# Kernel tuning notes

Hardware: AMD Instinct MI355X
Metric: run time of the kernel (lower is better)

## Reference

```python
import jax, jax.numpy as jnp
import numpy as np

NUM_EMBEDDINGS = 1024
EMBEDDING_DIM = 64
COMMITMENT_COST = 0.25


def setup_inputs() -> dict:
    key = jax.random.key(0)
    k1, k2 = jax.random.split(key)
    inputs = jax.random.normal(k1, (64, 32, 32, EMBEDDING_DIM), dtype=jnp.float32)
    embeddings = jax.random.normal(k2, (NUM_EMBEDDINGS, EMBEDDING_DIM), dtype=jnp.float32)
    return {"inputs": inputs, "embeddings": embeddings}


def reference(inputs, embeddings):
    # flatten spatial dims: [B, HW, D]
    flat = jnp.reshape(inputs, (inputs.shape[0], -1, EMBEDDING_DIM))
    distances = (
        jnp.sum(flat ** 2, axis=2, keepdims=True)
        - 2.0 * jnp.einsum("btd,kd->btk", flat, embeddings)
        + jnp.sum(embeddings ** 2, axis=1)
    )
    encoding_indices = jnp.argmin(distances, axis=2)  # [B, HW]
    # direct gather == one-hot @ embeddings, same math, no [B,HW,K] one-hot
    quantized = jnp.take(embeddings, encoding_indices, axis=0)  # [B, HW, D]
    quantized = jnp.reshape(quantized, inputs.shape)
    e_latent_loss = jnp.mean((jax.lax.stop_gradient(quantized) - inputs) ** 2)
    loss = COMMITMENT_COST * e_latent_loss
    quantized = inputs + jax.lax.stop_gradient(quantized - inputs)
    return quantized, loss, encoding_indices
```

## Files before the change

### kernel.cpp

```cpp
#include <hip/hip_runtime.h>

#define D 64
#define NK 1024
#define QTOTAL 65536
#define NELEM (QTOTAL * D)
#define LOSS_OFF 4194304
#define IDX_OUT_OFF 4194305
#define CAPQ 16384
#define MARGIN 2.0e-3f

typedef float f32x16 __attribute__((ext_vector_type(16)));
typedef short bf16x8 __attribute__((ext_vector_type(8)));
typedef float f32x4 __attribute__((ext_vector_type(4)));
typedef unsigned int u32;
typedef unsigned short ushort_t;

#define WS_E2   0
#define WS_B    4096
#define WS_CNT  266240
#define WS_LIST 266496
#define WS_NEED 332032

__device__ __forceinline__ ushort_t f2bf(float f) {
    u32 u = __float_as_uint(f);
    return (ushort_t)((u + 0x7FFFu + ((u >> 16) & 1u)) >> 16);
}
__device__ __forceinline__ float bf2f(ushort_t h) {
    return __uint_as_float(((u32)h) << 16);
}

__global__ __launch_bounds__(256) void vqk0(const float* __restrict__ emb,
                                            u32* __restrict__ b32,
                                            float* __restrict__ e2, u32* __restrict__ cnt,
                                            float* __restrict__ out) {
    int gid = blockIdx.x * 256 + threadIdx.x;
    int c = gid >> 5;
    int d = (gid & 31) * 2;
    float2 v = ((const float2*)emb)[gid];
    ushort_t h0 = f2bf(v.x), h1 = f2bf(v.y);
    ushort_t m0 = f2bf(v.x - bf2f(h0)), m1 = f2bf(v.y - bf2f(h1));
    int t = c >> 4, row = c & 15;
    int g = (d & 31) >> 3;
    int bh = (d < 32) ? 0 : 1;
    int lane = g * 16 + row;
    int u = t * 1024 + lane * 4 + ((d & 7) >> 1);
    b32[u + bh * 256]       = (u32)h0 | ((u32)h1 << 16);
    b32[u + (bh + 2) * 256] = (u32)m0 | ((u32)m1 << 16);
    if (gid < NK) {
        const float4* e4 = (const float4*)(emb + (long)gid * D);
        float s = 0.f;
#pragma unroll
        for (int i = 0; i < D / 4; ++i) {
            float4 w = e4[i];
            s += w.x * w.x + w.y * w.y + w.z * w.z + w.w * w.w;
        }
        e2[gid] = s;
    }
    if (gid == 0) { out[LOSS_OFF] = 0.0f; *cnt = 0; }
}

#define LDB(P) (*(const bf16x8*)(P))

#define COMPUTE_TILE(T, BH0, BH1, BM0, BM1) do {                               \
    const int c_ = (T) * 16 + row;                                             \
    const float h_ = 0.5f * e2l[c_];                                           \
    _Pragma("unroll")                                                          \
    for (int s_ = 0; s_ < 2; ++s_) {                                           \
        f32x4 acc = {0.f, 0.f, 0.f, 0.f};                                      \
        acc = __builtin_amdgcn_mfma_f32_16x16x32_bf16(ah[s_][0], BM0, acc, 0, 0, 0); \
        acc = __builtin_amdgcn_mfma_f32_16x16x32_bf16(am[s_][0], BH0, acc, 0, 0, 0); \
        acc = __builtin_amdgcn_mfma_f32_16x16x32_bf16(ah[s_][0], BH0, acc, 0, 0, 0); \
        acc = __builtin_amdgcn_mfma_f32_16x16x32_bf16(ah[s_][1], BM1, acc, 0, 0, 0); \
        acc = __builtin_amdgcn_mfma_f32_16x16x32_bf16(am[s_][1], BH1, acc, 0, 0, 0); \
        acc = __builtin_amdgcn_mfma_f32_16x16x32_bf16(ah[s_][1], BH1, acc, 0, 0, 0); \
        _Pragma("unroll")                                                      \
        for (int r_ = 0; r_ < 4; ++r_) {                                       \
            int sl_ = s_ * 4 + r_;                                             \
            float sd_ = h_ - acc[r_];                                          \
            float ns2_ = fminf(fmaxf(sd_, s1v[sl_]), s2v[sl_]);      \
            bool lt_ = sd_ < s1v[sl_];                                         \
            i1v[sl_] = lt_ ? c_ : i1v[sl_];                                    \
            s1v[sl_] = fminf(sd_, s1v[sl_]);                                   \
            s2v[sl_] = ns2_;                                                   \
        }                                                                      \
    }                                                                          \
} while (0)

__global__ __launch_bounds__(256, 2) void vqk1(const float* __restrict__ x,
                                               const ushort_t* __restrict__ B,
                                               const float* __restrict__ e2g,
                                               const float* __restrict__ emb,
                                               u32* __restrict__ cnt,
                                               int* __restrict__ list,
                                               float* __restrict__ out) {
    __shared__ float e2l[NK];
    __shared__ int   idx_l[128];
    __shared__ float lred[4];

    const int tid = threadIdx.x;
    const int l = tid & 63;
    const int w = tid >> 6;
    const int qbase = blockIdx.x * 128;
    const int wb = qbase + w * 32;
    const int row = l & 15;
    const int g = l >> 4;
    const int koff = g * 8;

    ((f32x4*)e2l)[tid] = ((const f32x4*)e2g)[tid];

    bf16x8 ah[2][2], am[2][2];
#pragma unroll
    for (int s = 0; s < 2; ++s) {
        const float* xr = x + (long)(wb + s * 16 + row) * D + koff;
#pragma unroll
        for (int half = 0; half < 2; ++half) {
            float4 p0 = ((const float4*)(xr + half * 32))[0];
            float4 p1 = ((const float4*)(xr + half * 32))[1];
            float v[8] = {p0.x, p0.y, p0.z, p0.w, p1.x, p1.y, p1.z, p1.w};
#pragma unroll
            for (int i = 0; i < 8; ++i) {
                ushort_t hs = f2bf(v[i]);
                ushort_t ms = f2bf(v[i] - bf2f(hs));
                ah[s][half][i] = (short)hs;
                am[s][half][i] = (short)ms;
            }
        }
    }
    __syncthreads();

    float s1v[8], s2v[8];
    int i1v[8];
#pragma unroll
    for (int i = 0; i < 8; ++i) { s1v[i] = 3.4e38f; s2v[i] = 3.4e38f; i1v[i] = 0; }

    int off = l * 8;
    bf16x8 bh0 = LDB(B + off),        bh1 = LDB(B + off + 512);
    bf16x8 bm0 = LDB(B + off + 1024), bm1 = LDB(B + off + 1536);
#pragma unroll 1
    for (int t = 0; t < 64; t += 2) {
        int o1 = off + 2048;
        bf16x8 ch0 = LDB(B + o1),        ch1 = LDB(B + o1 + 512);
        bf16x8 cm0 = LDB(B + o1 + 1024), cm1 = LDB(B + o1 + 1536);
        COMPUTE_TILE(t, bh0, bh1, bm0, bm1);
        int o2 = (t == 62) ? (l * 8) : (off + 4096);
        bh0 = LDB(B + o2);        bh1 = LDB(B + o2 + 512);
        bm0 = LDB(B + o2 + 1024); bm1 = LDB(B + o2 + 1536);
        COMPUTE_TILE(t + 1, ch0, ch1, cm0, cm1);
        off = o2;
    }

#pragma unroll
    for (int d = 1; d < 16; d <<= 1) {
#pragma unroll
        for (int sl = 0; sl < 8; ++sl) {
            float os1 = __shfl_xor(s1v[sl], d, 64);
            float os2 = __shfl_xor(s2v[sl], d, 64);
            int   oi1 = __shfl_xor(i1v[sl], d, 64);
            float hi = s1v[sl] > os1 ? s1v[sl] : os1;
            float lo2 = s2v[sl] < os2 ? s2v[sl] : os2;
            int ni = (os1 < s1v[sl]) ? oi1
                   : ((os1 == s1v[sl] && oi1 < i1v[sl]) ? oi1 : i1v[sl]);
            s1v[sl] = s1v[sl] < os1 ? s1v[sl] : os1;
            s2v[sl] = hi < lo2 ? hi : lo2;
            i1v[sl] = ni;
        }
    }

    if (row == 0) {
#pragma unroll
        for (int sl = 0; sl < 8; ++sl) {
            int s = sl >> 2, r = sl & 3;
            int ql = w * 32 + s * 16 + g * 4 + r;
            idx_l[ql] = i1v[sl];
            if (s2v[sl] - s1v[sl] <= MARGIN) {
                u32 p = atomicAdd(cnt, 1u);
                if (p < CAPQ) list[p] = qbase + ql;
            }
        }
    }
    __syncthreads();

    if (l < 32) out[IDX_OUT_OFF + wb + l] = (float)idx_l[w * 32 + l];

    const f32x4* x4 = (const f32x4*)(x + (long)wb * D);
    const f32x4* e4 = (const f32x4*)emb;
    f32x4* o4 = (f32x4*)(out + (long)wb * D);
    float ls = 0.f;
#pragma unroll 1
    for (int k = 0; k < 8; ++k) {
        int j = l + 64 * k;
        int ql = j >> 4;
        int col = j & 15;
        int idx = idx_l[w * 32 + ql];
        f32x4 xv = x4[j];
        f32x4 ev = e4[idx * 16 + col];
        o4[j] = ev;
        f32x4 dd = ev - xv;
        ls += dd[0] * dd[0] + dd[1] * dd[1] + dd[2] * dd[2] + dd[3] * dd[3];
    }
#pragma unroll
    for (int offr = 32; offr > 0; offr >>= 1) ls += __shfl_down(ls, offr, 64);
    if (l == 0) lred[w] = ls;
    __syncthreads();
    if (tid == 0)
        atomicAdd(&out[LOSS_OFF],
                  (lred[0] + lred[1] + lred[2] + lred[3]) * (0.25f / (float)NELEM));
}

__global__ __launch_bounds__(64) void vqk2(const float* __restrict__ x,
                                           const float* __restrict__ emb,
                                           const float* __restrict__ e2,
                                           const int* __restrict__ list,
                                           const u32* __restrict__ cnt,
                                           float* __restrict__ out) {
    u32 n = *cnt; if (n > CAPQ) n = CAPQ;
    const int l = threadIdx.x;
    for (u32 f = blockIdx.x; f < n; f += gridDim.x) {
        int q = list[f];
        float4 xv[16];
        const float4* xp = (const float4*)(x + (long)q * D);
#pragma unroll
        for (int i = 0; i < 16; ++i) xv[i] = xp[i];
        float best = 3.4e38f; int bi = 0;
#pragma unroll 1
        for (int i = 0; i < 16; ++i) {
            int c = l * 16 + i;
            const float4* ep = (const float4*)(emb + (long)c * D);
            float a0 = 0.f, a1 = 0.f, a2 = 0.f, a3 = 0.f;
#pragma unroll
            for (int k = 0; k < 16; ++k) {
                float4 e = ep[k];
                a0 = fmaf(e.x, xv[k].x, a0); a1 = fmaf(e.y, xv[k].y, a1);
                a2 = fmaf(e.z, xv[k].z, a2); a3 = fmaf(e.w, xv[k].w, a3);
            }
            float s = 0.5f * e2[c] - ((a0 + a1) + (a2 + a3));
            if (s < best) { best = s; bi = c; }
        }
#pragma unroll
        for (int off = 32; off > 0; off >>= 1) {
            float ob = __shfl_down(best, off, 64);
            int   oi = __shfl_down(bi, off, 64);
            if (ob < best || (ob == best && oi < bi)) { best = ob; bi = oi; }
        }
        bi = __shfl(bi, 0, 64);
        int ci = (int)out[IDX_OUT_OFF + q];
        if (bi != ci) {
            float xl = x[(long)q * D + l];
            float en = emb[(long)bi * D + l];
            float eo = emb[(long)ci * D + l];
            out[(long)q * D + l] = en;
            float dn = (en - xl) * (en - xl);
            float dol = (eo - xl) * (eo - xl);
            float dd = dn - dol;
#pragma unroll
            for (int off = 32; off > 0; off >>= 1) dd += __shfl_down(dd, off, 64);
            if (l == 0) {
                out[IDX_OUT_OFF + q] = (float)bi;
                atomicAdd(&out[LOSS_OFF], dd * (0.25f / (float)NELEM));
            }
        }
    }
}

#define FDO_CHUNK(B, K) \
    aA0 = fmaf(B[0],  xA[4*K+0].x, aA0); aA1 = fmaf(B[1],  xA[4*K+0].y, aA1); \
    aA2 = fmaf(B[2],  xA[4*K+0].z, aA2); aA3 = fmaf(B[3],  xA[4*K+0].w, aA3); \
    aA0 = fmaf(B[4],  xA[4*K+1].x, aA0); aA1 = fmaf(B[5],  xA[4*K+1].y, aA1); \
    aA2 = fmaf(B[6],  xA[4*K+1].z, aA2); aA3 = fmaf(B[7],  xA[4*K+1].w, aA3); \
    aA0 = fmaf(B[8],  xA[4*K+2].x, aA0); aA1 = fmaf(B[9],  xA[4*K+2].y, aA1); \
    aA2 = fmaf(B[10], xA[4*K+2].z, aA2); aA3 = fmaf(B[11], xA[4*K+2].w, aA3); \
    aA0 = fmaf(B[12], xA[4*K+3].x, aA0); aA1 = fmaf(B[13], xA[4*K+3].y, aA1); \
    aA2 = fmaf(B[14], xA[4*K+3].z, aA2); aA3 = fmaf(B[15], xA[4*K+3].w, aA3); \
    aB0 = fmaf(B[0],  xB[4*K+0].x, aB0); aB1 = fmaf(B[1],  xB[4*K+0].y, aB1); \
    aB2 = fmaf(B[2],  xB[4*K+0].z, aB2); aB3 = fmaf(B[3],  xB[4*K+0].w, aB3); \
    aB0 = fmaf(B[4],  xB[4*K+1].x, aB0); aB1 = fmaf(B[5],  xB[4*K+1].y, aB1); \
    aB2 = fmaf(B[6],  xB[4*K+1].z, aB2); aB3 = fmaf(B[7],  xB[4*K+1].w, aB3); \
    aB0 = fmaf(B[8],  xB[4*K+2].x, aB0); aB1 = fmaf(B[9],  xB[4*K+2].y, aB1); \
    aB2 = fmaf(B[10], xB[4*K+2].z, aB2); aB3 = fmaf(B[11], xB[4*K+2].w, aB3); \
    aB0 = fmaf(B[12], xB[4*K+3].x, aB0); aB1 = fmaf(B[13], xB[4*K+3].y, aB1); \
    aB2 = fmaf(B[14], xB[4*K+3].z, aB2); aB3 = fmaf(B[15], xB[4*K+3].w, aB3);

__global__ __launch_bounds__(256) void vq_e2f(const float* __restrict__ emb,
                                              float* __restrict__ e2,
                                              float* __restrict__ out) {
    int k = blockIdx.x * blockDim.x + threadIdx.x;
    if (k == 0) out[LOSS_OFF] = 0.0f;
    if (k < NK) {
        const float4* e4 = (const float4*)(emb + k * D);
        float s = 0.f;
#pragma unroll
        for (int i = 0; i < D / 4; ++i) {
            float4 v = e4[i];
            s += v.x * v.x + v.y * v.y + v.z * v.z + v.w * v.w;
        }
        e2[k] = s;
    }
}

__global__ __launch_bounds__(256, 2) void vq_mainf(const float* __restrict__ x,
                                                   const float* __restrict__ emb,
                                                   const float* __restrict__ e2g,
                                                   float* __restrict__ out) {
    __shared__ float e2l[NK];
    __shared__ float sm_s[512];
    __shared__ int   sm_c[512];
    const int tid = threadIdx.x;
    const int l = tid & 63;
    const int w = tid >> 6;
    const int qbase = blockIdx.x * 128;
    ((float4*)e2l)[tid] = ((const float4*)e2g)[tid];
    float4 xA[16], xB[16];
    const float4* xpA = (const float4*)(x + (long)(qbase + l) * D);
    const float4* xpB = (const float4*)(x + (long)(qbase + 64 + l) * D);
#pragma unroll
    for (int i = 0; i < 16; ++i) { xA[i] = xpA[i]; xB[i] = xpB[i]; }
    __syncthreads();
    const int code0 = __builtin_amdgcn_readfirstlane(w << 8);
    const float* ep0 = emb + (long)code0 * D;
    float bestA = 3.4e38f, bestB = 3.4e38f;
    int idxA = 0, idxB = 0;
#pragma unroll 1
    for (int g = 0; g < 256; ++g) {
        const float* ep = ep0 + g * D;
        f32x16 b0, b1, b2, b3;
        asm volatile(
            "s_load_dwordx16 %0, %4, 0x0\n\t"
            "s_load_dwordx16 %1, %4, 0x40\n\t"
            "s_load_dwordx16 %2, %4, 0x80\n\t"
            "s_load_dwordx16 %3, %4, 0xC0\n\t"
            "s_waitcnt lgkmcnt(0)"
            : "=s"(b0), "=s"(b1), "=s"(b2), "=s"(b3) : "s"(ep));
        float aA0 = 0.f, aA1 = 0.f, aA2 = 0.f, aA3 = 0.f;
        float aB0 = 0.f, aB1 = 0.f, aB2 = 0.f, aB3 = 0.f;
        FDO_CHUNK(b0, 0) FDO_CHUNK(b1, 1) FDO_CHUNK(b2, 2) FDO_CHUNK(b3, 3)
        float dotA = (aA0 + aA1) + (aA2 + aA3);
        float dotB = (aB0 + aB1) + (aB2 + aB3);
        float e2c = e2l[code0 + g];
        float sA = 0.5f * e2c - dotA;
        float sB = 0.5f * e2c - dotB;
        int code = code0 + g;
        bool lt;
        lt = sA < bestA; bestA = lt ? sA : bestA; idxA = lt ? code : idxA;
        lt = sB < bestB; bestB = lt ? sB : bestB; idxB = lt ? code : idxB;
    }
    sm_s[w * 128 + l] = bestA;      sm_c[w * 128 + l] = idxA;
    sm_s[w * 128 + 64 + l] = bestB; sm_c[w * 128 + 64 + l] = idxB;
    __syncthreads();
    if (tid < 128) {
        float bs = sm_s[tid]; int bc = sm_c[tid];
#pragma unroll
        for (int wv = 1; wv < 4; ++wv) {
            float s = sm_s[wv * 128 + tid]; int c = sm_c[wv * 128 + tid];
            if (s < bs) { bs = s; bc = c; }
        }
        const int q = qbase + tid;
        out[IDX_OUT_OFF + q] = (float)bc;
        const float4* eb = (const float4*)(emb + (long)bc * D);
        const float4* xq = (const float4*)(x + (long)q * D);
        float4* oq = (float4*)(out + (long)q * D);
        float lsum = 0.f;
#pragma unroll
        for (int i = 0; i < 16; ++i) {
            float4 e = eb[i]; float4 xx = xq[i];
            oq[i] = e;
            float dx = e.x - xx.x, dy = e.y - xx.y, dz = e.z - xx.z, dw = e.w - xx.w;
            lsum += dx * dx + dy * dy + dz * dz + dw * dw;
        }
#pragma unroll
        for (int o = 32; o > 0; o >>= 1) lsum += __shfl_down(lsum, o, 64);
        if ((tid & 63) == 0) atomicAdd(&out[LOSS_OFF], lsum * (0.25f / (float)NELEM));
    }
}

extern "C" void kernel_launch(void* const* d_in, const int* in_sizes, int n_in,
                              void* d_out, int out_size, void* d_ws, size_t ws_size,
                              hipStream_t stream) {
    const float* x   = (const float*)d_in[0];
    const float* emb = (const float*)d_in[1];
    float* out = (float*)d_out;
    char* ws = (char*)d_ws;

    if (ws_size < (size_t)WS_NEED) {
        float* e2 = (float*)ws;
        vq_e2f<<<4, 256, 0, stream>>>(emb, e2, out);
        vq_mainf<<<QTOTAL / 128, 256, 0, stream>>>(x, emb, e2, out);
        return;
    }

    float* e2    = (float*)(ws + WS_E2);
    ushort_t* B  = (ushort_t*)(ws + WS_B);
    u32* cnt     = (u32*)(ws + WS_CNT);
    int* list    = (int*)(ws + WS_LIST);

    vqk0<<<128, 256, 0, stream>>>(emb, (u32*)B, e2, cnt, out);
    vqk1<<<QTOTAL / 128, 256, 0, stream>>>(x, B, e2, emb, cnt, list, out);
    vqk2<<<256, 64, 0, stream>>>(x, emb, e2, list, cnt, out);
}
```

Measured before the change: 126.5 us.

## Stage codebook tiles through double-buffered LDS instead of per-wave global loads

Each block now cooperatively loads 4 codebook tiles at a time into a double-buffered shared-memory stage and feeds MFMA fragments from LDS, prefetching the next chunk from global while computing. Before, every wave loaded each B fragment from global/L2 on its own, so each block read the whole codebook four times. The 0.5 scale on the codebook norms is also folded into the one-time LDS fill. The cost is 32KB more LDS per block, which may limit occupancy, plus a block barrier every chunk.

```diff
diff --git a/kernel.cpp b/kernel.cpp
--- a/kernel.cpp
+++ b/kernel.cpp
@@ -59,11 +59,9 @@
     if (gid == 0) { out[LOSS_OFF] = 0.0f; *cnt = 0; }
 }
 
-#define LDB(P) (*(const bf16x8*)(P))
-
 #define COMPUTE_TILE(T, BH0, BH1, BM0, BM1) do {                               \
     const int c_ = (T) * 16 + row;                                             \
-    const float h_ = 0.5f * e2l[c_];                                           \
+    const float h_ = e2l[c_];                                                  \
     _Pragma("unroll")                                                          \
     for (int s_ = 0; s_ < 2; ++s_) {                                           \
         f32x4 acc = {0.f, 0.f, 0.f, 0.f};                                      \
@@ -86,6 +84,14 @@
     }                                                                          \
 } while (0)
 
+#define LDS_FRAG(SB, TT, H0, H1, M0, M1) do {                                  \
+    const ushort_t* p_ = (SB) + (TT) * 2048 + l * 8;                           \
+    H0 = *(const bf16x8*)(p_);                                                 \
+    H1 = *(const bf16x8*)(p_ + 512);                                           \
+    M0 = *(const bf16x8*)(p_ + 1024);                                          \
+    M1 = *(const bf16x8*)(p_ + 1536);                                          \
+} while (0)
+
 __global__ __launch_bounds__(256, 2) void vqk1(const float* __restrict__ x,
                                                const ushort_t* __restrict__ B,
                                                const float* __restrict__ e2g,
@@ -93,6 +99,7 @@
                                                u32* __restrict__ cnt,
                                                int* __restrict__ list,
                                                float* __restrict__ out) {
+    __shared__ f32x4 stage[2][1024];
     __shared__ float e2l[NK];
     __shared__ int   idx_l[128];
     __shared__ float lred[4];
@@ -106,7 +113,10 @@
     const int g = l >> 4;
     const int koff = g * 8;
 
-    ((f32x4*)e2l)[tid] = ((const f32x4*)e2g)[tid];
+    {
+        f32x4 t = ((const f32x4*)e2g)[tid];
+        ((f32x4*)e2l)[tid] = t * 0.5f;
+    }
 
     bf16x8 ah[2][2], am[2][2];
 #pragma unroll
@@ -126,27 +136,50 @@
             }
         }
     }
-    __syncthreads();
 
     float s1v[8], s2v[8];
     int i1v[8];
 #pragma unroll
     for (int i = 0; i < 8; ++i) { s1v[i] = 3.4e38f; s2v[i] = 3.4e38f; i1v[i] = 0; }
 
-    int off = l * 8;
-    bf16x8 bh0 = LDB(B + off),        bh1 = LDB(B + off + 512);
-    bf16x8 bm0 = LDB(B + off + 1024), bm1 = LDB(B + off + 1536);
+    const f32x4* gB = (const f32x4*)B;
+
+    {
+        f32x4 st0[4];
+#pragma unroll
+        for (int tt = 0; tt < 4; ++tt) st0[tt] = gB[tt * 256 + tid];
+#pragma unroll
+        for (int tt = 0; tt < 4; ++tt) stage[0][tt * 256 + tid] = st0[tt];
+    }
+    __syncthreads();
+
 #pragma unroll 1
-    for (int t = 0; t < 64; t += 2) {
-        int o1 = off + 2048;
-        bf16x8 ch0 = LDB(B + o1),        ch1 = LDB(B + o1 + 512);
-        bf16x8 cm0 = LDB(B + o1 + 1024), cm1 = LDB(B + o1 + 1536);
-        COMPUTE_TILE(t, bh0, bh1, bm0, bm1);
-        int o2 = (t == 62) ? (l * 8) : (off + 4096);
-        bh0 = LDB(B + o2);        bh1 = LDB(B + o2 + 512);
-        bm0 = LDB(B + o2 + 1024); bm1 = LDB(B + o2 + 1536);
-        COMPUTE_TILE(t + 1, ch0, ch1, cm0, cm1);
-        off = o2;
+    for (int c = 0; c < 16; ++c) {
+        const int cb = c & 1;
+        const ushort_t* sb = (const ushort_t*)&stage[cb][0];
+
+        f32x4 st[4];
+        if (c < 15) {
+#pragma unroll
+            for (int tt = 0; tt < 4; ++tt)
+                st[tt] = gB[(c + 1) * 1024 + tt * 256 + tid];
+        }
+
+        bf16x8 bh0, bh1, bm0, bm1, nh0, nh1, nm0, nm1;
+        LDS_FRAG(sb, 0, bh0, bh1, bm0, bm1);
+#pragma unroll
+        for (int tt = 0; tt < 4; ++tt) {
+            if (tt < 3) LDS_FRAG(sb, tt + 1, nh0, nh1, nm0, nm1);
+            COMPUTE_TILE(c * 4 + tt, bh0, bh1, bm0, bm1);
+            bh0 = nh0; bh1 = nh1; bm0 = nm0; bm1 = nm1;
+        }
+
+        if (c < 15) {
+#pragma unroll
+            for (int tt = 0; tt < 4; ++tt)
+                stage[cb ^ 1][tt * 256 + tid] = st[tt];
+        }
+        __syncthreads();
     }
 
 #pragma unroll
```

New measurement: 121.7 us. -3.8%, faster.
